# Performance work log

Measured on AMD Instinct MI355X. Metric: run time of the kernel, lower is better.

The kernel has to match this reference:

```python
import jax, jax.numpy as jnp
import numpy as np

N = 100000
E = 1600000
IN_C, HID_C, OUT_C = 128, 128, 64


def setup_inputs() -> dict:
    key = jax.random.key(0)
    ks = jax.random.split(key, 8)
    x = jax.random.normal(ks[0], (N, IN_C), dtype=jnp.float32)
    edge_index = jax.random.randint(ks[1], (2, E), 0, N, dtype=jnp.int64)

    def glorot(k, fan_in, fan_out):
        s = jnp.sqrt(6.0 / (fan_in + fan_out))
        return jax.random.uniform(k, (fan_in, fan_out), jnp.float32, -s, s)

    W1 = glorot(ks[2], IN_C, HID_C)
    b1 = jnp.zeros((HID_C,), jnp.float32)
    W2 = glorot(ks[3], HID_C, HID_C)
    b2 = jnp.zeros((HID_C,), jnp.float32)
    W3 = glorot(ks[4], HID_C, OUT_C)
    b3 = jnp.zeros((OUT_C,), jnp.float32)
    return {"x": x, "edge_index": edge_index,
            "W1": W1, "b1": b1, "W2": W2, "b2": b2, "W3": W3, "b3": b3}


def _gcn_norm(row, col, n_nodes):
    # symmetric normalization, add_self_loops=False (PyG gcn_norm)
    deg = jax.ops.segment_sum(jnp.ones(row.shape[0], jnp.float32), col, num_segments=n_nodes)
    dinv = jnp.where(deg > 0, jax.lax.rsqrt(jnp.maximum(deg, 1.0)), 0.0)
    dinv = jnp.where(deg > 0, deg ** -0.5, 0.0)
    return dinv[row] * dinv[col]  # [E]


def _gcn_conv(x, row, col, norm, W, b):
    h = x @ W                                # [N, F_out] dense GEMM first (PyG order)
    msg = h[row] * norm[:, None]             # gather + scale, [E, F_out]
    out = jax.ops.segment_sum(msg, col, num_segments=x.shape[0])  # scatter-add
    return out + b


def reference(x, edge_index, W1, b1, W2, b2, W3, b3):
    row, col = edge_index[0], edge_index[1]
    norm = _gcn_norm(row, col, x.shape[0])
    h = jax.nn.relu(_gcn_conv(x, row, col, norm, W1, b1))   # dropout is identity in eval
    h = jax.nn.relu(_gcn_conv(h, row, col, norm, W2, b2))
    out = _gcn_conv(h, row, col, norm, W3, b3)
    return out
```

## Files before the change

### kernel.cpp

```cpp
#include <hip/hip_runtime.h>
#include <hip/hip_bf16.h>
#include <hip/hip_fp16.h>


#define K_DIM 128
#define SCAN_CHUNK 1024

typedef _Float16 f16x8 __attribute__((ext_vector_type(8)));
typedef float f32x4 __attribute__((ext_vector_type(4)));

static inline long long cdiv_ll(long long a, long long b) { return (a + b - 1) / b; }

__global__ __launch_bounds__(256) void count_kernel(const int* __restrict__ col, int* __restrict__ cnt,
                                                    int* __restrict__ rank, int E) {
    int e = blockIdx.x * 256 + threadIdx.x;
    if (e < E) rank[e] = atomicAdd(&cnt[col[e]], 1);
}

__global__ __launch_bounds__(256) void dinv_kernel(const int* __restrict__ cnt, float* __restrict__ dinv, int N) {
    int n = blockIdx.x * 256 + threadIdx.x;
    if (n < N) {
        int d = cnt[n];
        dinv[n] = (d > 0) ? (1.0f / sqrtf((float)d)) : 0.0f;
    }
}

__global__ __launch_bounds__(256) void scan1_kernel(const int* __restrict__ cnt, int* __restrict__ off,
                                                    int* __restrict__ bsum, int N) {
    __shared__ int lds[256];
    const int t = threadIdx.x;
    const int base = blockIdx.x * SCAN_CHUNK;
    int v[4], s = 0;
#pragma unroll
    for (int j = 0; j < 4; ++j) {
        int i = base + t * 4 + j;
        v[j] = (i < N) ? cnt[i] : 0;
        s += v[j];
    }
    lds[t] = s;
    __syncthreads();
    for (int d = 1; d < 256; d <<= 1) {
        int x = (t >= d) ? lds[t - d] : 0;
        __syncthreads();
        lds[t] += x;
        __syncthreads();
    }
    int excl = lds[t] - s;
    if (t == 255) bsum[blockIdx.x] = lds[255];
    int run = excl;
#pragma unroll
    for (int j = 0; j < 4; ++j) {
        int i = base + t * 4 + j;
        if (i < N) off[i] = run;
        run += v[j];
    }
}

__global__ __launch_bounds__(256) void scan2_kernel(int* __restrict__ bsum, int G, int* __restrict__ off,
                                                    int N, int E) {
    __shared__ int lds[256];
    const int t = threadIdx.x;
    int s = (t < G) ? bsum[t] : 0;
    lds[t] = s;
    __syncthreads();
    for (int d = 1; d < 256; d <<= 1) {
        int x = (t >= d) ? lds[t - d] : 0;
        __syncthreads();
        lds[t] += x;
        __syncthreads();
    }
    if (t < G) bsum[t] = lds[t] - s;
    if (t == 0) off[N] = E;
}

__global__ __launch_bounds__(256) void scan3_kernel(int* __restrict__ off, const int* __restrict__ bsum, int N) {
    int add = bsum[blockIdx.x];
    const int base = blockIdx.x * SCAN_CHUNK;
#pragma unroll
    for (int j = 0; j < 4; ++j) {
        int i = base + threadIdx.x * 4 + j;
        if (i < N) off[i] += add;
    }
}

__global__ __launch_bounds__(256) void fill_kernel(const int* __restrict__ row, const int* __restrict__ col,
                                                   const int* __restrict__ off, const int* __restrict__ rank,
                                                   int* __restrict__ csr_row, int E) {
    int e = blockIdx.x * 256 + threadIdx.x;
    if (e < E) {
        int idx = off[col[e]] + rank[e];
        __builtin_nontemporal_store(row[e], &csr_row[idx]);
    }
}

template <int COUT>
__global__ __launch_bounds__(256) void pack_w_kernel(const float* __restrict__ W, _Float16* __restrict__ Wp) {
    constexpr int NT = COUT / 16;
    int t = blockIdx.x * 256 + threadIdx.x;
    if (t >= 4 * NT * 64) return;
    int lane = t & 63;
    int nt = (t >> 6) % NT;
    int kt = t / (64 * NT);
    int c = lane & 15, q = lane >> 4;
    f16x8 v;
#pragma unroll
    for (int j = 0; j < 8; ++j) {
        int k = kt * 32 + q * 8 + j;
        v[j] = (_Float16)W[k * COUT + nt * 16 + c];
    }
    *(f16x8*)&Wp[(size_t)t * 8] = v;
}

template <int COUT, bool AF16>
__global__ __launch_bounds__(256) void gemm_mfma(const void* __restrict__ Av, const _Float16* __restrict__ Wp,
                                                 const float* __restrict__ dinv, _Float16* __restrict__ Cmat, int M) {
    constexpr int NT = COUT / 16;
    constexpr int NFRAG = 4 * NT * 64;
    __shared__ _Float16 Wlds[NFRAG * 8];

    const int t = threadIdx.x;
    for (int i = t; i < NFRAG; i += 256)
        *(f16x8*)&Wlds[(size_t)i * 8] = *(const f16x8*)&Wp[(size_t)i * 8];
    __syncthreads();

    const int lane = t & 63;
    const int wave = t >> 6;
    const int c = lane & 15;
    const int q = lane >> 4;
    const int row_base = blockIdx.x * 128 + wave * 32;

    f32x4 acc[2][NT];
#pragma unroll
    for (int rt = 0; rt < 2; ++rt)
#pragma unroll
        for (int nt = 0; nt < NT; ++nt) {
            acc[rt][nt][0] = 0.f; acc[rt][nt][1] = 0.f;
            acc[rt][nt][2] = 0.f; acc[rt][nt][3] = 0.f;
        }

#pragma unroll
    for (int kt = 0; kt < 4; ++kt) {
        f16x8 a[2];
#pragma unroll
        for (int rt = 0; rt < 2; ++rt) {
            int r = row_base + rt * 16 + c;
            r = (r < M) ? r : (M - 1);
            if (AF16) {
                a[rt] = *(const f16x8*)((const _Float16*)Av + (size_t)r * K_DIM + kt * 32 + q * 8);
            } else {
                const float* ap = (const float*)Av + (size_t)r * K_DIM + kt * 32 + q * 8;
                float4 v0 = *(const float4*)ap;
                float4 v1 = *(const float4*)(ap + 4);
                f16x8 av;
                av[0] = (_Float16)v0.x; av[1] = (_Float16)v0.y;
                av[2] = (_Float16)v0.z; av[3] = (_Float16)v0.w;
                av[4] = (_Float16)v1.x; av[5] = (_Float16)v1.y;
                av[6] = (_Float16)v1.z; av[7] = (_Float16)v1.w;
                a[rt] = av;
            }
        }
#pragma unroll
        for (int nt = 0; nt < NT; ++nt) {
            f16x8 b = *(const f16x8*)&Wlds[(size_t)((kt * NT + nt) * 64 + lane) * 8];
            acc[0][nt] = __builtin_amdgcn_mfma_f32_16x16x32_f16(a[0], b, acc[0][nt], 0, 0, 0);
            acc[1][nt] = __builtin_amdgcn_mfma_f32_16x16x32_f16(a[1], b, acc[1][nt], 0, 0, 0);
        }
    }

#pragma unroll
    for (int rt = 0; rt < 2; ++rt)
#pragma unroll
        for (int reg = 0; reg < 4; ++reg) {
            int row = row_base + rt * 16 + q * 4 + reg;
            if (row < M) {
                float dv = dinv[row];
#pragma unroll
                for (int nt = 0; nt < NT; ++nt)
                    Cmat[(size_t)row * COUT + nt * 16 + c] = (_Float16)(acc[rt][nt][reg] * dv);
            }
        }
}

template <int C, bool RELU, typename OutT>
__global__ __launch_bounds__(256) void gather_row(const _Float16* __restrict__ g, const int* __restrict__ off,
                                                  const int* __restrict__ csr_row, const float* __restrict__ dinv,
                                                  const float* __restrict__ bias, OutT* __restrict__ outp, int N) {
    constexpr int SUBS = C / 8;
    constexpr int LOG_SUBS = (SUBS == 16) ? 4 : 3;
    constexpr int NTILE = 256 / SUBS;
    constexpr int CH = 96;
    constexpr int RST = C + 8;
    __shared__ __align__(16) _Float16 feat[CH * RST];
    __shared__ int off_s[NTILE + 1];

    const int t = threadIdx.x;
    const int node0 = blockIdx.x * NTILE;

    if (t <= NTILE) {
        int idx = node0 + t;
        off_s[t] = off[idx < N ? idx : N];
    }
    __syncthreads();

    const int n_loc = t >> LOG_SUBS;
    const int sub = t & (SUBS - 1);
    const int node = node0 + n_loc;
    const bool valid = node < N;
    const int sn0 = off_s[n_loc];
    const int sn1 = off_s[n_loc + 1];
    const int s_begin = off_s[0];
    const int s_end = off_s[NTILE];

    float acc[8];
#pragma unroll
    for (int k = 0; k < 8; ++k) acc[k] = 0.f;

    for (int cs = s_begin; cs < s_end; cs += CH) {
        const int ce = (cs + CH < s_end) ? (cs + CH) : s_end;
        const int cnt = ce - cs;
        const int units = cnt << LOG_SUBS;
        for (int u = t; u < units; u += 256) {
            int rloc = u >> LOG_SUBS;
            int seg = u & (SUBS - 1);
            int r = csr_row[cs + rloc];
            f16x8 v = *(const f16x8*)(g + (size_t)r * C + seg * 8);
            *(f16x8*)&feat[rloc * RST + seg * 8] = v;
        }
        __syncthreads();
        const int lo_s = (sn0 > cs) ? sn0 : cs;
        const int hi_s = (sn1 < ce) ? sn1 : ce;
        const _Float16* fb = &feat[sub * 8];
        for (int s = lo_s; s < hi_s; ++s) {
            f16x8 v = *(const f16x8*)&fb[(s - cs) * RST];
#pragma unroll
            for (int k = 0; k < 8; ++k) acc[k] += (float)v[k];
        }
        __syncthreads();
    }

    if (valid) {
        const float dv = dinv[node];
        const float* bp = bias + sub * 8;
        float o[8];
#pragma unroll
        for (int k = 0; k < 8; ++k) {
            o[k] = acc[k] * dv + bp[k];
            if (RELU) o[k] = fmaxf(o[k], 0.f);
        }
        if constexpr (sizeof(OutT) == 2) {
            f16x8 ov;
#pragma unroll
            for (int k = 0; k < 8; ++k) ov[k] = (_Float16)o[k];
            *(f16x8*)((_Float16*)outp + (size_t)node * C + sub * 8) = ov;
        } else {
            float* op = (float*)outp + (size_t)node * C + sub * 8;
            *(float4*)op = make_float4(o[0], o[1], o[2], o[3]);
            *(float4*)(op + 4) = make_float4(o[4], o[5], o[6], o[7]);
        }
    }
}

extern "C" void kernel_launch(void* const* d_in, const int* in_sizes, int n_in,
                              void* d_out, int out_size, void* d_ws, size_t ws_size,
                              hipStream_t stream) {
    const float* x  = (const float*)d_in[0];
    const int*   ei = (const int*)d_in[1];
    const float* W1 = (const float*)d_in[2];
    const float* b1 = (const float*)d_in[3];
    const float* W2 = (const float*)d_in[4];
    const float* b2 = (const float*)d_in[5];
    const float* W3 = (const float*)d_in[6];
    const float* b3 = (const float*)d_in[7];

    const int N = in_sizes[0] / 128;
    const int E = in_sizes[1] / 2;
    const int* row = ei;
    const int* col = ei + E;
    const int G = (int)cdiv_ll(N, SCAN_CHUNK);

    char* wsb = (char*)d_ws;
    int*      cnt     = (int*)wsb;      wsb += (size_t)N * 4;
    float*    dinv    = (float*)wsb;    wsb += (size_t)N * 4;
    int*      off     = (int*)wsb;      wsb += (size_t)(N + 1) * 4;
    int*      bsum    = (int*)wsb;      wsb += 256 * 4;
    int*      rank    = (int*)wsb;      wsb += (size_t)E * 4;
    int*      csr_row = (int*)wsb;      wsb += (size_t)E * 4;
    wsb = (char*)((((uintptr_t)wsb) + 15) & ~(uintptr_t)15);
    _Float16* Wp1     = (_Float16*)wsb; wsb += 16384 * 2;
    _Float16* Wp2     = (_Float16*)wsb; wsb += 16384 * 2;
    _Float16* Wp3     = (_Float16*)wsb; wsb += 8192 * 2;
    _Float16* bufA    = (_Float16*)wsb; wsb += (size_t)N * 128 * 2;
    _Float16* bufB    = (_Float16*)wsb;
    float*    out     = (float*)d_out;

    hipMemsetAsync(cnt, 0, (size_t)N * 4, stream);
    count_kernel<<<cdiv_ll(E, 256), 256, 0, stream>>>(col, cnt, rank, E);
    dinv_kernel<<<cdiv_ll(N, 256), 256, 0, stream>>>(cnt, dinv, N);
    scan1_kernel<<<G, 256, 0, stream>>>(cnt, off, bsum, N);
    scan2_kernel<<<1, 256, 0, stream>>>(bsum, G, off, N, E);
    scan3_kernel<<<G, 256, 0, stream>>>(off, bsum, N);
    fill_kernel<<<cdiv_ll(E, 256), 256, 0, stream>>>(row, col, off, rank, csr_row, E);
    pack_w_kernel<128><<<8, 256, 0, stream>>>(W1, Wp1);
    pack_w_kernel<128><<<8, 256, 0, stream>>>(W2, Wp2);
    pack_w_kernel<64><<<4, 256, 0, stream>>>(W3, Wp3);

    const long long gemmBlocks = cdiv_ll(N, 128);
    const long long g128Blocks = cdiv_ll(N, 16);
    const long long g64Blocks  = cdiv_ll(N, 32);

    gemm_mfma<128, false><<<gemmBlocks, 256, 0, stream>>>(x, Wp1, dinv, bufA, N);
    gather_row<128, true, _Float16><<<g128Blocks, 256, 0, stream>>>(bufA, off, csr_row, dinv, b1, bufB, N);

    gemm_mfma<128, true><<<gemmBlocks, 256, 0, stream>>>(bufB, Wp2, dinv, bufA, N);
    gather_row<128, true, _Float16><<<g128Blocks, 256, 0, stream>>>(bufA, off, csr_row, dinv, b2, bufB, N);

    gemm_mfma<64, true><<<gemmBlocks, 256, 0, stream>>>(bufB, Wp3, dinv, bufA, N);
    gather_row<64, false, float><<<g64Blocks, 256, 0, stream>>>(bufA, off, csr_row, dinv, b3, out, N);
}
```

Baseline: 520.2 us.

## Software-pipeline gather staging through registers and fuse small setup kernels

The gather kernel now loads the next chunk of neighbor features into registers while the current LDS chunk is reduced, then commits them to LDS. This double-buffering hides global gather latency behind the accumulation. LDS padding is replaced with a rotating (swizzled) segment layout to avoid bank conflicts, and chunk sizes shrink to fit the register staging. The dinv computation is folded into scan1 and the three weight-pack kernels are merged into one launch, cutting launch overhead at the cost of higher register pressure in the gather.

```diff
diff --git a/kernel.cpp b/kernel.cpp
--- a/kernel.cpp
+++ b/kernel.cpp
@@ -17,16 +17,8 @@
     if (e < E) rank[e] = atomicAdd(&cnt[col[e]], 1);
 }
 
-__global__ __launch_bounds__(256) void dinv_kernel(const int* __restrict__ cnt, float* __restrict__ dinv, int N) {
-    int n = blockIdx.x * 256 + threadIdx.x;
-    if (n < N) {
-        int d = cnt[n];
-        dinv[n] = (d > 0) ? (1.0f / sqrtf((float)d)) : 0.0f;
-    }
-}
-
 __global__ __launch_bounds__(256) void scan1_kernel(const int* __restrict__ cnt, int* __restrict__ off,
-                                                    int* __restrict__ bsum, int N) {
+                                                    int* __restrict__ bsum, float* __restrict__ dinv, int N) {
     __shared__ int lds[256];
     const int t = threadIdx.x;
     const int base = blockIdx.x * SCAN_CHUNK;
@@ -35,6 +27,7 @@
     for (int j = 0; j < 4; ++j) {
         int i = base + t * 4 + j;
         v[j] = (i < N) ? cnt[i] : 0;
+        if (i < N) dinv[i] = (v[j] > 0) ? (1.0f / sqrtf((float)v[j])) : 0.0f;
         s += v[j];
     }
     lds[t] = s;
@@ -94,9 +87,8 @@
 }
 
 template <int COUT>
-__global__ __launch_bounds__(256) void pack_w_kernel(const float* __restrict__ W, _Float16* __restrict__ Wp) {
+__device__ __forceinline__ void pack_body(const float* __restrict__ W, _Float16* __restrict__ Wp, int t) {
     constexpr int NT = COUT / 16;
-    int t = blockIdx.x * 256 + threadIdx.x;
     if (t >= 4 * NT * 64) return;
     int lane = t & 63;
     int nt = (t >> 6) % NT;
@@ -109,6 +101,15 @@
         v[j] = (_Float16)W[k * COUT + nt * 16 + c];
     }
     *(f16x8*)&Wp[(size_t)t * 8] = v;
+}
+
+__global__ __launch_bounds__(256) void pack_all_kernel(const float* __restrict__ W1, const float* __restrict__ W2,
+                                                       const float* __restrict__ W3, _Float16* __restrict__ Wp1,
+                                                       _Float16* __restrict__ Wp2, _Float16* __restrict__ Wp3) {
+    int b = blockIdx.x;
+    if (b < 8)       pack_body<128>(W1, Wp1, b * 256 + threadIdx.x);
+    else if (b < 16) pack_body<128>(W2, Wp2, (b - 8) * 256 + threadIdx.x);
+    else             pack_body<64>(W3, Wp3, (b - 16) * 256 + threadIdx.x);
 }
 
 template <int COUT, bool AF16>
@@ -182,15 +183,15 @@
 }
 
 template <int C, bool RELU, typename OutT>
-__global__ __launch_bounds__(256) void gather_row(const _Float16* __restrict__ g, const int* __restrict__ off,
-                                                  const int* __restrict__ csr_row, const float* __restrict__ dinv,
-                                                  const float* __restrict__ bias, OutT* __restrict__ outp, int N) {
+__global__ __launch_bounds__(256) void gather_pipe(const _Float16* __restrict__ g, const int* __restrict__ off,
+                                                   const int* __restrict__ csr_row, const float* __restrict__ dinv,
+                                                   const float* __restrict__ bias, OutT* __restrict__ outp, int N) {
     constexpr int SUBS = C / 8;
-    constexpr int LOG_SUBS = (SUBS == 16) ? 4 : 3;
+    constexpr int LS = (SUBS == 16) ? 4 : 3;
     constexpr int NTILE = 256 / SUBS;
-    constexpr int CH = 96;
-    constexpr int RST = C + 8;
-    __shared__ __align__(16) _Float16 feat[CH * RST];
+    constexpr int CH = (C == 128) ? 48 : 64;
+    constexpr int UPT = CH * SUBS / 256;
+    __shared__ __align__(16) _Float16 feat[CH * C];
     __shared__ int off_s[NTILE + 1];
 
     const int t = threadIdx.x;
@@ -202,7 +203,7 @@
     }
     __syncthreads();
 
-    const int n_loc = t >> LOG_SUBS;
+    const int n_loc = t >> LS;
     const int sub = t & (SUBS - 1);
     const int node = node0 + n_loc;
     const bool valid = node < N;
@@ -215,27 +216,57 @@
 #pragma unroll
     for (int k = 0; k < 8; ++k) acc[k] = 0.f;
 
-    for (int cs = s_begin; cs < s_end; cs += CH) {
-        const int ce = (cs + CH < s_end) ? (cs + CH) : s_end;
-        const int cnt = ce - cs;
-        const int units = cnt << LOG_SUBS;
-        for (int u = t; u < units; u += 256) {
-            int rloc = u >> LOG_SUBS;
-            int seg = u & (SUBS - 1);
-            int r = csr_row[cs + rloc];
-            f16x8 v = *(const f16x8*)(g + (size_t)r * C + seg * 8);
-            *(f16x8*)&feat[rloc * RST + seg * 8] = v;
-        }
-        __syncthreads();
-        const int lo_s = (sn0 > cs) ? sn0 : cs;
-        const int hi_s = (sn1 < ce) ? sn1 : ce;
-        const _Float16* fb = &feat[sub * 8];
-        for (int s = lo_s; s < hi_s; ++s) {
-            f16x8 v = *(const f16x8*)&fb[(s - cs) * RST];
-#pragma unroll
-            for (int k = 0; k < 8; ++k) acc[k] += (float)v[k];
-        }
-        __syncthreads();
+    f16x8 stg[UPT];
+
+    auto stage = [&](int cs) {
+        int ce = (cs + CH < s_end) ? (cs + CH) : s_end;
+        int units = (ce - cs) << LS;
+#pragma unroll
+        for (int i = 0; i < UPT; ++i) {
+            int u = t + i * 256;
+            if (u < units) {
+                int rloc = u >> LS;
+                int slot = u & (SUBS - 1);
+                int seg = (slot - rloc) & (SUBS - 1);
+                int r = csr_row[cs + rloc];
+                stg[i] = *(const f16x8*)(g + (size_t)r * C + seg * 8);
+            }
+        }
+    };
+    auto commit = [&](int cs) {
+        int ce = (cs + CH < s_end) ? (cs + CH) : s_end;
+        int units = (ce - cs) << LS;
+#pragma unroll
+        for (int i = 0; i < UPT; ++i) {
+            int u = t + i * 256;
+            if (u < units) *(f16x8*)&feat[u * 8] = stg[i];
+        }
+    };
+
+    if (s_begin < s_end) {
+        stage(s_begin);
+        commit(s_begin);
+        __syncthreads();
+        for (int cs = s_begin; cs < s_end; cs += CH) {
+            const int nxt = cs + CH;
+            const bool more = nxt < s_end;
+            if (more) stage(nxt);
+            const int ce = more ? nxt : s_end;
+            const int lo_s = (sn0 > cs) ? sn0 : cs;
+            const int hi_s = (sn1 < ce) ? sn1 : ce;
+            for (int s = lo_s; s < hi_s; ++s) {
+                int rl = s - cs;
+                int slot = (sub + rl) & (SUBS - 1);
+                f16x8 v = *(const f16x8*)&feat[rl * C + slot * 8];
+#pragma unroll
+                for (int k = 0; k < 8; ++k) acc[k] += (float)v[k];
+            }
+            __syncthreads();
+            if (more) {
+                commit(nxt);
+                __syncthreads();
+            }
+        }
     }
 
     if (valid) {
@@ -295,25 +326,22 @@
 
     hipMemsetAsync(cnt, 0, (size_t)N * 4, stream);
     count_kernel<<<cdiv_ll(E, 256), 256, 0, stream>>>(col, cnt, rank, E);
-    dinv_kernel<<<cdiv_ll(N, 256), 256, 0, stream>>>(cnt, dinv, N);
-    scan1_kernel<<<G, 256, 0, stream>>>(cnt, off, bsum, N);
+    scan1_kernel<<<G, 256, 0, stream>>>(cnt, off, bsum, dinv, N);
     scan2_kernel<<<1, 256, 0, stream>>>(bsum, G, off, N, E);
     scan3_kernel<<<G, 256, 0, stream>>>(off, bsum, N);
     fill_kernel<<<cdiv_ll(E, 256), 256, 0, stream>>>(row, col, off, rank, csr_row, E);
-    pack_w_kernel<128><<<8, 256, 0, stream>>>(W1, Wp1);
-    pack_w_kernel<128><<<8, 256, 0, stream>>>(W2, Wp2);
-    pack_w_kernel<64><<<4, 256, 0, stream>>>(W3, Wp3);
+    pack_all_kernel<<<20, 256, 0, stream>>>(W1, W2, W3, Wp1, Wp2, Wp3);
 
     const long long gemmBlocks = cdiv_ll(N, 128);
     const long long g128Blocks = cdiv_ll(N, 16);
     const long long g64Blocks  = cdiv_ll(N, 32);
 
     gemm_mfma<128, false><<<gemmBlocks, 256, 0, stream>>>(x, Wp1, dinv, bufA, N);
-    gather_row<128, true, _Float16><<<g128Blocks, 256, 0, stream>>>(bufA, off, csr_row, dinv, b1, bufB, N);
+    gather_pipe<128, true, _Float16><<<g128Blocks, 256, 0, stream>>>(bufA, off, csr_row, dinv, b1, bufB, N);
 
     gemm_mfma<128, true><<<gemmBlocks, 256, 0, stream>>>(bufB, Wp2, dinv, bufA, N);
-    gather_row<128, true, _Float16><<<g128Blocks, 256, 0, stream>>>(bufA, off, csr_row, dinv, b2, bufB, N);
+    gather_pipe<128, true, _Float16><<<g128Blocks, 256, 0, stream>>>(bufA, off, csr_row, dinv, b2, bufB, N);
 
     gemm_mfma<64, true><<<gemmBlocks, 256, 0, stream>>>(bufB, Wp3, dinv, bufA, N);
-    gather_row<64, false, float><<<g64Blocks, 256, 0, stream>>>(bufA, off, csr_row, dinv, b3, out, N);
-}
+    gather_pipe<64, false, float><<<g64Blocks, 256, 0, stream>>>(bufA, off, csr_row, dinv, b3, out, N);
+}
```

New measurement: 503.3 us. -3.2%, faster.
